# Kernel optimization log

Measured on AMD Instinct MI355X. Metric: run time of the kernel, lower is better.

Reference implementation:

```python
import jax, jax.numpy as jnp
import numpy as np

N_NODES = 100000
D_IN, D_OUT = 1024, 512
B, K = 8192, 64


def setup_inputs() -> dict:
    key = jax.random.key(0)
    k1, k2, k3, k4, k5 = jax.random.split(key, 5)
    X = jax.random.normal(k1, (N_NODES, D_IN), dtype=jnp.float32)
    indices = jax.random.randint(k2, (B, K), 0, N_NODES)  # top-K PPR neighbor ids per batch node
    values = jax.random.uniform(k3, (B, K), dtype=jnp.float32)  # PPR weights
    W = jax.random.normal(k4, (D_IN, D_OUT), dtype=jnp.float32) / np.sqrt(D_IN)
    b = jax.random.normal(k5, (D_OUT,), dtype=jnp.float32)
    return {"X": X, "indices": indices, "values": values, "W": W, "b": b}


def reference(X, indices, values, W, b):
    # Sparse PPR branch. Original: encode only unique gathered rows, then
    # re-expand via inverse indices. Since the encoder is row-pointwise,
    # encoder(X[u_fwd])[u_bwd] == encoder(X)[indices]; we encode all nodes once
    # (n_nodes < B*K here) then gather -- identical math, jit-friendly.
    enc = X @ W + b                      # [N, d_out]
    gathered = enc[indices]              # [B, K, d_out]
    return jnp.einsum('bk,bkd->bd', values, gathered)  # weighted sum over K neighbors
```

## Files before the change

### kernel.cpp

```cpp
#include <hip/hip_runtime.h>

typedef unsigned short ushort_t;
typedef __bf16 bf16x8 __attribute__((ext_vector_type(8)));
typedef float f32x4 __attribute__((ext_vector_type(4)));

#define N_NODES 100000
#define D_IN    1024
#define D_OUT   512
#define B_SZ    8192
#define K_NB    64

__device__ __forceinline__ ushort_t f2bf(float f) {
    unsigned int u = __builtin_bit_cast(unsigned int, f);
    u += 0x7FFFu + ((u >> 16) & 1u);
    return (ushort_t)(u >> 16);
}
__device__ __forceinline__ float bflo(unsigned d) {
    return __builtin_bit_cast(float, d << 16);
}
__device__ __forceinline__ float bfhi(unsigned d) {
    return __builtin_bit_cast(float, d & 0xFFFF0000u);
}

__global__ __launch_bounds__(256) void cast_w_kernel(
        const float* __restrict__ W, ushort_t* __restrict__ Wt) {
    int o = blockIdx.x * 256 + threadIdx.x;
    int n = o >> 10;
    int k = o & 1023;
    Wt[o] = f2bf(W[k * D_OUT + n]);
}

__global__ __launch_bounds__(256) void cast_x_kernel(
        const float* __restrict__ X, ushort_t* __restrict__ Xb) {
    size_t o = ((size_t)blockIdx.x * 256 + threadIdx.x) * 8;
    float4 a = *(const float4*)(X + o);
    float4 b = *(const float4*)(X + o + 4);
    uint4 r;
    r.x = (unsigned)f2bf(a.x) | ((unsigned)f2bf(a.y) << 16);
    r.y = (unsigned)f2bf(a.z) | ((unsigned)f2bf(a.w) << 16);
    r.z = (unsigned)f2bf(b.x) | ((unsigned)f2bf(b.y) << 16);
    r.w = (unsigned)f2bf(b.z) | ((unsigned)f2bf(b.w) << 16);
    *(uint4*)(Xb + o) = r;
}

__global__ __launch_bounds__(256) void gather_bf16_kernel(
        const ushort_t* __restrict__ Xb, const int* __restrict__ idx,
        const float* __restrict__ val, ushort_t* __restrict__ Y,
        float* __restrict__ s) {
    int b = blockIdx.x;
    int t = threadIdx.x;

    __shared__ int   sidx[K_NB];
    __shared__ float sval[K_NB];
    __shared__ float part[128 * 8];
    if (t < K_NB) {
        sidx[t] = idx[b * K_NB + t];
        sval[t] = val[b * K_NB + t];
    }
    __syncthreads();

    int h = t >> 7;
    int c = t & 127;

    float acc[8] = {0.f, 0.f, 0.f, 0.f, 0.f, 0.f, 0.f, 0.f};

    uint4 x[8];
    #pragma unroll
    for (int u = 0; u < 8; u++)
        x[u] = ((const uint4*)(Xb + (size_t)sidx[h + 2 * u] * D_IN))[c];

    #pragma unroll
    for (int j0 = 0; j0 < 32; j0 += 8) {
        uint4 cur[8];
        #pragma unroll
        for (int u = 0; u < 8; u++) cur[u] = x[u];
        if (j0 + 8 < 32) {
            #pragma unroll
            for (int u = 0; u < 8; u++)
                x[u] = ((const uint4*)(
                    Xb + (size_t)sidx[h + 2 * (j0 + 8 + u)] * D_IN))[c];
        }
        #pragma unroll
        for (int u = 0; u < 8; u++) {
            float v = sval[h + 2 * (j0 + u)];
            acc[0] = fmaf(v, bflo(cur[u].x), acc[0]);
            acc[1] = fmaf(v, bfhi(cur[u].x), acc[1]);
            acc[2] = fmaf(v, bflo(cur[u].y), acc[2]);
            acc[3] = fmaf(v, bfhi(cur[u].y), acc[3]);
            acc[4] = fmaf(v, bflo(cur[u].z), acc[4]);
            acc[5] = fmaf(v, bfhi(cur[u].z), acc[5]);
            acc[6] = fmaf(v, bflo(cur[u].w), acc[6]);
            acc[7] = fmaf(v, bfhi(cur[u].w), acc[7]);
        }
    }

    if (h == 1) {
        #pragma unroll
        for (int e = 0; e < 8; e++) part[c * 8 + e] = acc[e];
    }
    __syncthreads();
    if (h == 0) {
        ushort_t r[8];
        #pragma unroll
        for (int e = 0; e < 8; e++) r[e] = f2bf(acc[e] + part[c * 8 + e]);
        uint4 o;
        o.x = (unsigned)r[0] | ((unsigned)r[1] << 16);
        o.y = (unsigned)r[2] | ((unsigned)r[3] << 16);
        o.z = (unsigned)r[4] | ((unsigned)r[5] << 16);
        o.w = (unsigned)r[6] | ((unsigned)r[7] << 16);
        *(uint4*)(Y + (size_t)b * D_IN + c * 8) = o;
    }
    if (t == 0) {
        float sum = 0.f;
        #pragma unroll
        for (int k = 0; k < K_NB; k++) sum += sval[k];
        s[b] = sum;
    }
}

__global__ __launch_bounds__(256) void gather_f32_kernel(
        const float* __restrict__ X, const int* __restrict__ idx,
        const float* __restrict__ val, ushort_t* __restrict__ Y,
        float* __restrict__ s) {
    int b = blockIdx.x;
    int t = threadIdx.x;

    __shared__ int   sidx[K_NB];
    __shared__ float sval[K_NB];
    if (t < K_NB) {
        sidx[t] = idx[b * K_NB + t];
        sval[t] = val[b * K_NB + t];
    }
    __syncthreads();

    float ax = 0.f, ay = 0.f, az = 0.f, aw = 0.f;
    #pragma unroll 8
    for (int k = 0; k < K_NB; k++) {
        const float4* row = (const float4*)(X + (size_t)sidx[k] * D_IN);
        float4 x = row[t];
        float  v = sval[k];
        ax = fmaf(v, x.x, ax);
        ay = fmaf(v, x.y, ay);
        az = fmaf(v, x.z, az);
        aw = fmaf(v, x.w, aw);
    }
    uint2 o;
    o.x = (unsigned)f2bf(ax) | ((unsigned)f2bf(ay) << 16);
    o.y = (unsigned)f2bf(az) | ((unsigned)f2bf(aw) << 16);
    *(uint2*)(Y + (size_t)b * D_IN + t * 4) = o;

    if (t == 0) {
        float sum = 0.f;
        #pragma unroll
        for (int k = 0; k < K_NB; k++) sum += sval[k];
        s[b] = sum;
    }
}

__global__ __launch_bounds__(256) void gemm_kernel(
        const ushort_t* __restrict__ Y, const ushort_t* __restrict__ Wt,
        const float* __restrict__ s, const float* __restrict__ bias,
        float* __restrict__ out) {
    const int Kdim = D_IN;
    int m0 = blockIdx.x * 128;
    int n0 = blockIdx.y * 128;
    int t = threadIdx.x;
    int lane = t & 63;
    int wave = t >> 6;
    int wm = (wave >> 1) * 64;
    int wn = (wave & 1) * 64;
    int quad = lane >> 4;
    int l16  = lane & 15;

    __shared__ __align__(16) ushort_t As[128 * 32];
    __shared__ __align__(16) ushort_t Bs[128 * 32];

    f32x4 acc[4][4];
    f32x4 zero = {0.f, 0.f, 0.f, 0.f};
    #pragma unroll
    for (int i = 0; i < 4; i++)
        #pragma unroll
        for (int j = 0; j < 4; j++)
            acc[i][j] = zero;

    int rsw = (l16 >> 2) & 3;

    for (int k0 = 0; k0 < Kdim; k0 += 32) {
        #pragma unroll
        for (int i = 0; i < 2; i++) {
            int c   = t + i * 256;
            int row = c >> 2;
            int chk = c & 3;
            int pos = chk ^ ((row >> 2) & 3);
            *(int4*)(As + row * 32 + pos * 8) =
                *(const int4*)(Y + (size_t)(m0 + row) * Kdim + k0 + chk * 8);
            *(int4*)(Bs + row * 32 + pos * 8) =
                *(const int4*)(Wt + (size_t)(n0 + row) * Kdim + k0 + chk * 8);
        }
        __syncthreads();

        bf16x8 a[4], b[4];
        int rchk = quad ^ rsw;
        #pragma unroll
        for (int i = 0; i < 4; i++) {
            a[i] = *(const bf16x8*)(As + (wm + i * 16 + l16) * 32 + rchk * 8);
            b[i] = *(const bf16x8*)(Bs + (wn + i * 16 + l16) * 32 + rchk * 8);
        }
        #pragma unroll
        for (int i = 0; i < 4; i++)
            #pragma unroll
            for (int j = 0; j < 4; j++)
                acc[i][j] = __builtin_amdgcn_mfma_f32_16x16x32_bf16(
                                a[i], b[j], acc[i][j], 0, 0, 0);
        __syncthreads();
    }

    #pragma unroll
    for (int i = 0; i < 4; i++) {
        #pragma unroll
        for (int r = 0; r < 4; r++) {
            int grow = m0 + wm + i * 16 + quad * 4 + r;
            float sv = s[grow];
            #pragma unroll
            for (int j = 0; j < 4; j++) {
                int gcol = n0 + wn + j * 16 + l16;
                out[(size_t)grow * D_OUT + gcol] = acc[i][j][r] + sv * bias[gcol];
            }
        }
    }
}

extern "C" void kernel_launch(void* const* d_in, const int* in_sizes, int n_in,
                              void* d_out, int out_size, void* d_ws, size_t ws_size,
                              hipStream_t stream) {
    const float* X    = (const float*)d_in[0];
    const int*   idx  = (const int*)d_in[1];
    const float* val  = (const float*)d_in[2];
    const float* W    = (const float*)d_in[3];
    const float* bias = (const float*)d_in[4];
    float* out = (float*)d_out;

    const size_t XB_BYTES = (size_t)N_NODES * D_IN * 2;
    const size_t Y_BYTES  = (size_t)B_SZ * D_IN * 2;
    const size_t WT_BYTES = (size_t)D_OUT * D_IN * 2;
    const size_t S_BYTES  = (size_t)B_SZ * 4;

    char* ws = (char*)d_ws;
    bool fast = ws_size >= XB_BYTES + Y_BYTES + WT_BYTES + S_BYTES;

    ushort_t *Xb, *Yb, *Wt;
    float *sb;
    if (fast) {
        Xb = (ushort_t*)ws;
        Yb = (ushort_t*)(ws + XB_BYTES);
        Wt = (ushort_t*)(ws + XB_BYTES + Y_BYTES);
        sb = (float*)(ws + XB_BYTES + Y_BYTES + WT_BYTES);
    } else {
        Xb = nullptr;
        Yb = (ushort_t*)ws;
        Wt = (ushort_t*)(ws + Y_BYTES);
        sb = (float*)(ws + Y_BYTES + WT_BYTES);
    }

    hipLaunchKernelGGL(cast_w_kernel, dim3((D_OUT * D_IN) / 256), dim3(256),
                       0, stream, W, Wt);
    if (fast) {
        hipLaunchKernelGGL(cast_x_kernel, dim3((N_NODES * D_IN) / (256 * 8)),
                           dim3(256), 0, stream, X, Xb);
        hipLaunchKernelGGL(gather_bf16_kernel, dim3(B_SZ), dim3(256),
                           0, stream, Xb, idx, val, Yb, sb);
    } else {
        hipLaunchKernelGGL(gather_f32_kernel, dim3(B_SZ), dim3(256),
                           0, stream, X, idx, val, Yb, sb);
    }
    hipLaunchKernelGGL(gemm_kernel, dim3(B_SZ / 128, D_OUT / 128), dim3(256),
                       0, stream, Yb, Wt, sb, bias, out);
}
```

Before: 731.6 us.

## Encode all nodes with a bf16 MFMA GEMM, then gather encoded rows

The order of operations is reversed. All padded node rows are first encoded with a bf16 MFMA GEMM that loads global memory straight into LDS and folds the bias into a bf16 encoding buffer. A per-batch gather then reads 512-wide encoded rows and writes the weighted fp32 output directly. The aim is to halve the bytes moved by the large K=64 random gather and to drop the intermediate Y buffer and the row-sum pass. The cost is a much larger GEMM over 100k rows instead of 8192, a bigger workspace requirement, and an extra bf16 rounding of the encoded values before the weighted sum.

```diff
diff --git a/kernel.cpp b/kernel.cpp
--- a/kernel.cpp
+++ b/kernel.cpp
@@ -5,6 +5,7 @@
 typedef float f32x4 __attribute__((ext_vector_type(4)));
 
 #define N_NODES 100000
+#define M_PAD   100096
 #define D_IN    1024
 #define D_OUT   512
 #define B_SZ    8192
@@ -20,6 +21,13 @@
 }
 __device__ __forceinline__ float bfhi(unsigned d) {
     return __builtin_bit_cast(float, d & 0xFFFF0000u);
+}
+
+__device__ __forceinline__ void gload16(const ushort_t* g, ushort_t* l) {
+    __builtin_amdgcn_global_load_lds(
+        (const __attribute__((address_space(1))) void*)g,
+        (__attribute__((address_space(3))) void*)l,
+        16, 0, 0);
 }
 
 __global__ __launch_bounds__(256) void cast_w_kernel(
@@ -43,46 +51,117 @@
     *(uint4*)(Xb + o) = r;
 }
 
-__global__ __launch_bounds__(256) void gather_bf16_kernel(
-        const ushort_t* __restrict__ Xb, const int* __restrict__ idx,
-        const float* __restrict__ val, ushort_t* __restrict__ Y,
-        float* __restrict__ s) {
+__global__ __launch_bounds__(256) void encode_gemm_kernel(
+        const ushort_t* __restrict__ Xb, const ushort_t* __restrict__ Wt,
+        const float* __restrict__ bias, ushort_t* __restrict__ Enc) {
+    int m0 = blockIdx.x * 128;
+    int n0 = blockIdx.y * 128;
+    int t = threadIdx.x;
+    int lane = t & 63;
+    int wave = t >> 6;
+    int wm = (wave >> 1) * 64;
+    int wn = (wave & 1) * 64;
+    int quad = lane >> 4;
+    int l16  = lane & 15;
+
+    __shared__ __align__(16) ushort_t As[128 * 32];
+    __shared__ __align__(16) ushort_t Bs[128 * 32];
+
+    f32x4 acc[4][4];
+    f32x4 zero = {0.f, 0.f, 0.f, 0.f};
+    #pragma unroll
+    for (int i = 0; i < 4; i++)
+        #pragma unroll
+        for (int j = 0; j < 4; j++)
+            acc[i][j] = zero;
+
+    const ushort_t* ga = Xb + (size_t)(m0 + (t >> 2)) * D_IN + (t & 3) * 8;
+    const ushort_t* gb = Wt + (size_t)(n0 + (t >> 2)) * D_IN + (t & 3) * 8;
+    ushort_t* la = As + t * 8;
+    ushort_t* lb = Bs + t * 8;
+    const size_t rowskip = (size_t)64 * D_IN;
+
+    for (int k0 = 0; k0 < D_IN; k0 += 32) {
+        gload16(ga + k0,           la);
+        gload16(ga + rowskip + k0, la + 2048);
+        gload16(gb + k0,           lb);
+        gload16(gb + rowskip + k0, lb + 2048);
+        __syncthreads();
+
+        bf16x8 a[4], b[4];
+        #pragma unroll
+        for (int i = 0; i < 4; i++) {
+            a[i] = *(const bf16x8*)(As + (wm + i * 16 + l16) * 32 + quad * 8);
+            b[i] = *(const bf16x8*)(Bs + (wn + i * 16 + l16) * 32 + quad * 8);
+        }
+        #pragma unroll
+        for (int i = 0; i < 4; i++)
+            #pragma unroll
+            for (int j = 0; j < 4; j++)
+                acc[i][j] = __builtin_amdgcn_mfma_f32_16x16x32_bf16(
+                                a[i], b[j], acc[i][j], 0, 0, 0);
+        __syncthreads();
+    }
+
+    float bv[4];
+    #pragma unroll
+    for (int j = 0; j < 4; j++) bv[j] = bias[n0 + wn + j * 16 + l16];
+
+    #pragma unroll
+    for (int i = 0; i < 4; i++) {
+        #pragma unroll
+        for (int r = 0; r < 4; r++) {
+            int grow = m0 + wm + i * 16 + quad * 4 + r;
+            if (grow < N_NODES) {
+                #pragma unroll
+                for (int j = 0; j < 4; j++) {
+                    int gcol = n0 + wn + j * 16 + l16;
+                    Enc[(size_t)grow * D_OUT + gcol] = f2bf(acc[i][j][r] + bv[j]);
+                }
+            }
+        }
+    }
+}
+
+__global__ __launch_bounds__(256) void gather_out_kernel(
+        const ushort_t* __restrict__ Enc, const int* __restrict__ idx,
+        const float* __restrict__ val, float* __restrict__ out) {
     int b = blockIdx.x;
     int t = threadIdx.x;
 
     __shared__ int   sidx[K_NB];
     __shared__ float sval[K_NB];
-    __shared__ float part[128 * 8];
+    __shared__ float part[8 * 3 * 64];
     if (t < K_NB) {
         sidx[t] = idx[b * K_NB + t];
         sval[t] = val[b * K_NB + t];
     }
     __syncthreads();
 
-    int h = t >> 7;
-    int c = t & 127;
+    int h = t >> 6;
+    int c = t & 63;
 
     float acc[8] = {0.f, 0.f, 0.f, 0.f, 0.f, 0.f, 0.f, 0.f};
 
     uint4 x[8];
     #pragma unroll
     for (int u = 0; u < 8; u++)
-        x[u] = ((const uint4*)(Xb + (size_t)sidx[h + 2 * u] * D_IN))[c];
-
-    #pragma unroll
-    for (int j0 = 0; j0 < 32; j0 += 8) {
+        x[u] = ((const uint4*)(Enc + (size_t)sidx[h + 4 * u] * D_OUT))[c];
+
+    #pragma unroll
+    for (int j0 = 0; j0 < 16; j0 += 8) {
         uint4 cur[8];
         #pragma unroll
         for (int u = 0; u < 8; u++) cur[u] = x[u];
-        if (j0 + 8 < 32) {
+        if (j0 + 8 < 16) {
             #pragma unroll
             for (int u = 0; u < 8; u++)
                 x[u] = ((const uint4*)(
-                    Xb + (size_t)sidx[h + 2 * (j0 + 8 + u)] * D_IN))[c];
+                    Enc + (size_t)sidx[h + 4 * (j0 + 8 + u)] * D_OUT))[c];
         }
         #pragma unroll
         for (int u = 0; u < 8; u++) {
-            float v = sval[h + 2 * (j0 + u)];
+            float v = sval[h + 4 * (j0 + u)];
             acc[0] = fmaf(v, bflo(cur[u].x), acc[0]);
             acc[1] = fmaf(v, bfhi(cur[u].x), acc[1]);
             acc[2] = fmaf(v, bflo(cur[u].y), acc[2]);
@@ -94,27 +173,23 @@
         }
     }
 
-    if (h == 1) {
-        #pragma unroll
-        for (int e = 0; e < 8; e++) part[c * 8 + e] = acc[e];
+    if (h != 0) {
+        #pragma unroll
+        for (int e = 0; e < 8; e++)
+            part[e * 192 + (h - 1) * 64 + c] = acc[e];
     }
     __syncthreads();
     if (h == 0) {
-        ushort_t r[8];
-        #pragma unroll
-        for (int e = 0; e < 8; e++) r[e] = f2bf(acc[e] + part[c * 8 + e]);
-        uint4 o;
-        o.x = (unsigned)r[0] | ((unsigned)r[1] << 16);
-        o.y = (unsigned)r[2] | ((unsigned)r[3] << 16);
-        o.z = (unsigned)r[4] | ((unsigned)r[5] << 16);
-        o.w = (unsigned)r[6] | ((unsigned)r[7] << 16);
-        *(uint4*)(Y + (size_t)b * D_IN + c * 8) = o;
-    }
-    if (t == 0) {
-        float sum = 0.f;
-        #pragma unroll
-        for (int k = 0; k < K_NB; k++) sum += sval[k];
-        s[b] = sum;
+        float r[8];
+        #pragma unroll
+        for (int e = 0; e < 8; e++)
+            r[e] = acc[e] + part[e * 192 + c] + part[e * 192 + 64 + c]
+                          + part[e * 192 + 128 + c];
+        float4 o0 = {r[0], r[1], r[2], r[3]};
+        float4 o1 = {r[4], r[5], r[6], r[7]};
+        float* dst = out + (size_t)b * D_OUT + c * 8;
+        *(float4*)(dst)     = o0;
+        *(float4*)(dst + 4) = o1;
     }
 }
 
@@ -240,39 +315,38 @@
     const float* bias = (const float*)d_in[4];
     float* out = (float*)d_out;
 
-    const size_t XB_BYTES = (size_t)N_NODES * D_IN * 2;
-    const size_t Y_BYTES  = (size_t)B_SZ * D_IN * 2;
-    const size_t WT_BYTES = (size_t)D_OUT * D_IN * 2;
-    const size_t S_BYTES  = (size_t)B_SZ * 4;
+    const size_t XB_BYTES  = (size_t)M_PAD * D_IN * 2;
+    const size_t ENC_BYTES = (size_t)M_PAD * D_OUT * 2;
+    const size_t WT_BYTES  = (size_t)D_OUT * D_IN * 2;
+    const size_t Y_BYTES   = (size_t)B_SZ * D_IN * 2;
+    const size_t S_BYTES   = (size_t)B_SZ * 4;
 
     char* ws = (char*)d_ws;
-    bool fast = ws_size >= XB_BYTES + Y_BYTES + WT_BYTES + S_BYTES;
-
-    ushort_t *Xb, *Yb, *Wt;
-    float *sb;
+    bool fast = ws_size >= XB_BYTES + ENC_BYTES + WT_BYTES;
+
     if (fast) {
-        Xb = (ushort_t*)ws;
-        Yb = (ushort_t*)(ws + XB_BYTES);
-        Wt = (ushort_t*)(ws + XB_BYTES + Y_BYTES);
-        sb = (float*)(ws + XB_BYTES + Y_BYTES + WT_BYTES);
-    } else {
-        Xb = nullptr;
-        Yb = (ushort_t*)ws;
-        Wt = (ushort_t*)(ws + Y_BYTES);
-        sb = (float*)(ws + Y_BYTES + WT_BYTES);
-    }
-
-    hipLaunchKernelGGL(cast_w_kernel, dim3((D_OUT * D_IN) / 256), dim3(256),
-                       0, stream, W, Wt);
-    if (fast) {
+        ushort_t* Xb  = (ushort_t*)ws;
+        ushort_t* Enc = (ushort_t*)(ws + XB_BYTES);
+        ushort_t* Wt  = (ushort_t*)(ws + XB_BYTES + ENC_BYTES);
+
+        hipLaunchKernelGGL(cast_w_kernel, dim3((D_OUT * D_IN) / 256), dim3(256),
+                           0, stream, W, Wt);
         hipLaunchKernelGGL(cast_x_kernel, dim3((N_NODES * D_IN) / (256 * 8)),
                            dim3(256), 0, stream, X, Xb);
-        hipLaunchKernelGGL(gather_bf16_kernel, dim3(B_SZ), dim3(256),
-                           0, stream, Xb, idx, val, Yb, sb);
+        hipLaunchKernelGGL(encode_gemm_kernel, dim3(M_PAD / 128, D_OUT / 128),
+                           dim3(256), 0, stream, Xb, Wt, bias, Enc);
+        hipLaunchKernelGGL(gather_out_kernel, dim3(B_SZ), dim3(256),
+                           0, stream, Enc, idx, val, out);
     } else {
+        ushort_t* Yb = (ushort_t*)ws;
+        ushort_t* Wt = (ushort_t*)(ws + Y_BYTES);
+        float*    sb = (float*)(ws + Y_BYTES + WT_BYTES);
+
+        hipLaunchKernelGGL(cast_w_kernel, dim3((D_OUT * D_IN) / 256), dim3(256),
+                           0, stream, W, Wt);
         hipLaunchKernelGGL(gather_f32_kernel, dim3(B_SZ), dim3(256),
                            0, stream, X, idx, val, Yb, sb);
-    }
-    hipLaunchKernelGGL(gemm_kernel, dim3(B_SZ / 128, D_OUT / 128), dim3(256),
-                       0, stream, Yb, Wt, sb, bias, out);
-}
+        hipLaunchKernelGGL(gemm_kernel, dim3(B_SZ / 128, D_OUT / 128), dim3(256),
+                           0, stream, Yb, Wt, sb, bias, out);
+    }
+}
```

Measured after the change: 801.8 us. 1.1x slower.
